# Kernel optimization log

Measured on AMD Instinct MI355X. Metric: run time of the kernel, lower is better.

The kernel has to match this reference:

```python
import jax, jax.numpy as jnp
import numpy as np
import math

V, TB, C, H, L = 50257, 1024, 1024, 16, 8
B, T = 2, 1024
D = C // H


def setup_inputs() -> dict:
    key = jax.random.key(0)
    ks = jax.random.split(key, 16)
    s = 0.02
    n = lambda k, shp: (jax.random.normal(k, shp, jnp.float32) * s)
    inp = {
        "idx": jax.random.randint(ks[0], (B, T), 0, V),
        "tok_emb": n(ks[1], (V, C)),
        "pos_emb": n(ks[2], (1, TB, C)),
        # per-layer stacked params (torch Linear convention: W is [out, in])
        "Wq": n(ks[3], (L, C, C)), "bq": jnp.zeros((L, C)),
        "Wk": n(ks[4], (L, C, C)), "bk": jnp.zeros((L, C)),
        "Wv": n(ks[5], (L, C, C)), "bv": jnp.zeros((L, C)),
        "Wp": n(ks[6], (L, C, C)), "bp": jnp.zeros((L, C)),
        "ln1_w": jnp.ones((L, C)), "ln1_b": jnp.zeros((L, C)),
        "ln2_w": jnp.ones((L, C)), "ln2_b": jnp.zeros((L, C)),
        "W1": n(ks[7], (L, 4 * C, C)), "b1": jnp.zeros((L, 4 * C)),
        "W2": n(ks[8], (L, C, 4 * C)), "b2": jnp.zeros((L, C)),
        "lnf_w": jnp.ones((C,)), "lnf_b": jnp.zeros((C,)),
        "head_w": n(ks[9], (V, C)),
    }
    return inp


def _layer_norm(x, w, b, eps=1e-5):
    mu = x.mean(-1, keepdims=True)
    var = x.var(-1, keepdims=True)
    return (x - mu) * jax.lax.rsqrt(var + eps) * w + b


def _gpt_forward(idx, tok_emb, pos_emb, Wq, bq, Wk, bk, Wv, bv, Wp, bp,
                 ln1_w, ln1_b, ln2_w, ln2_b, W1, b1, W2, b2, lnf_w, lnf_b, head_w):
    b, t = idx.shape
    x = tok_emb[idx] + pos_emb[:, :t, :]  # [B, T, C]; drop = identity (eval)
    causal = jnp.tril(jnp.ones((t, t), dtype=bool))  # [T, T]
    scale = 1.0 / math.sqrt(D)

    def block(x, p):
        (wq, bq_, wk, bk_, wv, bv_, wp, bp_, l1w, l1b, l2w, l2b, w1, b1_, w2, b2_) = p
        h = _layer_norm(x, l1w, l1b)
        q = (h @ wq.T + bq_).reshape(b, t, H, D).transpose(0, 2, 1, 3)  # [B,H,T,D]
        k = (h @ wk.T + bk_).reshape(b, t, H, D).transpose(0, 2, 1, 3)
        v = (h @ wv.T + bv_).reshape(b, t, H, D).transpose(0, 2, 1, 3)
        att = jnp.einsum("bhqd,bhkd->bhqk", q, k) * scale
        att = jnp.where(causal, att, -jnp.inf)
        att = jax.nn.softmax(att, axis=-1)
        y = jnp.einsum("bhqk,bhkd->bhqd", att, v)
        y = y.transpose(0, 2, 1, 3).reshape(b, t, C)
        x = x + (y @ wp.T + bp_)
        h2 = _layer_norm(x, l2w, l2b)
        m = jax.nn.gelu(h2 @ w1.T + b1_, approximate=False)  # torch nn.GELU (erf)
        x = x + (m @ w2.T + b2_)
        return x, None

    params = (Wq, bq, Wk, bk, Wv, bv, Wp, bp, ln1_w, ln1_b, ln2_w, ln2_b, W1, b1, W2, b2)
    x, _ = jax.lax.scan(block, x, params)
    x = _layer_norm(x, lnf_w, lnf_b)
    logits = x @ head_w.T  # [B, T, V]
    return logits


def reference(idx, tok_emb, pos_emb, Wq, bq, Wk, bk, Wv, bv, Wp, bp,
              ln1_w, ln1_b, ln2_w, ln2_b, W1, b1, W2, b2, lnf_w, lnf_b, head_w):
    return _gpt_forward(idx, tok_emb, pos_emb, Wq, bq, Wk, bk, Wv, bv, Wp, bp,
                        ln1_w, ln1_b, ln2_w, ln2_b, W1, b1, W2, b2, lnf_w, lnf_b, head_w)
```

## Files before the change

### kernel.cpp

```cpp
#include <hip/hip_runtime.h>
#include <math.h>

#define V_ 50257
#define C_ 1024
#define H_ 16
#define L_ 8
#define B_ 2
#define T_ 1024
#define BT_ 2048
#define CC_ (C_*C_)
#define QLD_ 3072

typedef unsigned short ushort_t;
using bf16x8 = __attribute__((ext_vector_type(8))) short;
using f32x4  = __attribute__((ext_vector_type(4))) float;

#define AS1 __attribute__((address_space(1)))
#define AS3 __attribute__((address_space(3)))
#define VMCNT0() asm volatile("s_waitcnt vmcnt(0)" ::: "memory")
#define LGKM0()  asm volatile("s_waitcnt lgkmcnt(0)" ::: "memory")
#define RBAR()   asm volatile("s_barrier" ::: "memory")

__device__ __forceinline__ ushort_t f2bf(float f){
  union { float f; unsigned u; } a; a.f = f;
  unsigned r = a.u + 0x7fffu + ((a.u >> 16) & 1u);
  return (ushort_t)(r >> 16);
}

__device__ __forceinline__ unsigned cvtpk_bf16(float a, float b){
  unsigned r;
  asm("v_cvt_pk_bf16_f32 %0, %1, %2" : "=v"(r) : "v"(a), "v"(b));
  return r;
}

__device__ __forceinline__ float wave_sum(float v){
  #pragma unroll
  for(int o=32;o>0;o>>=1) v += __shfl_down(v,o,64);
  return v;
}

__global__ __launch_bounds__(256) void cvt_blk(const float* __restrict__ s, ushort_t* __restrict__ d,
    long inner4, int nblk, long dstStride4){
  long total = inner4 * nblk;
  for(long i = (long)blockIdx.x*256 + threadIdx.x; i < total; i += (long)gridDim.x*256){
    long blk = i / inner4, r = i - blk*inner4;
    float4 v = ((const float4*)s)[i];
    ushort4 o; o.x=f2bf(v.x); o.y=f2bf(v.y); o.z=f2bf(v.z); o.w=f2bf(v.w);
    ((ushort4*)d)[blk*dstStride4 + r] = o;
  }
}

__global__ __launch_bounds__(256) void cvt_qkv(const float* __restrict__ wq,
    const float* __restrict__ wk, const float* __restrict__ wv, ushort_t* __restrict__ d){
  const long inner4 = (long)CC_/4;
  const long total = (long)L_*3*inner4;
  for(long i = (long)blockIdx.x*256 + threadIdx.x; i < total; i += (long)gridDim.x*256){
    long l = i / (3*inner4), r = i - l*3*inner4;
    int which = (int)(r / inner4);
    long rr = r - (long)which*inner4;
    const float* s = (which==0 ? wq : which==1 ? wk : wv) + (l*inner4 + rr)*4;
    float4 v = *(const float4*)s;
    ushort4 o; o.x=f2bf(v.x); o.y=f2bf(v.y); o.z=f2bf(v.z); o.w=f2bf(v.w);
    ((ushort4*)d)[i] = o;
  }
}

__global__ __launch_bounds__(256) void pack_qkv_bias(const float* __restrict__ bq,
    const float* __restrict__ bk, const float* __restrict__ bv, float* __restrict__ dst){
  int i = blockIdx.x*256 + threadIdx.x;
  int l = i / QLD_, c = i - l*QLD_;
  float v;
  if(c < C_)            v = bq[l*C_ + c];
  else if(c < 2*C_)     v = bk[l*C_ + c - C_];
  else                  v = bv[l*C_ + c - 2*C_];
  dst[i] = v;
}

__global__ __launch_bounds__(256) void embed_kernel(const int* __restrict__ idx,
    const float* __restrict__ tok, const float* __restrict__ pos, float* __restrict__ x){
  int i = blockIdx.x*256 + threadIdx.x;
  int c = i & (C_-1); int bt = i >> 10; int t = bt & (T_-1);
  x[i] = tok[(size_t)idx[bt]*C_ + c] + pos[t*C_ + c];
}

__global__ __launch_bounds__(256) void ln_kernel(const float* in, const float* __restrict__ w,
    const float* __restrict__ b, float* outF, ushort_t* outB){
  int row = blockIdx.x;
  const float* xr = in + (size_t)row*C_;
  float vals[4]; float sum=0.f, sq=0.f;
  #pragma unroll
  for(int l=0;l<4;l++){ float v = xr[threadIdx.x + l*256]; vals[l]=v; sum+=v; sq+=v*v; }
  __shared__ float r1[4], r2[4];
  float s1 = wave_sum(sum), s2 = wave_sum(sq);
  int wid = threadIdx.x>>6, lane = threadIdx.x&63;
  if(lane==0){ r1[wid]=s1; r2[wid]=s2; }
  __syncthreads();
  float tot  = r1[0]+r1[1]+r1[2]+r1[3];
  float tot2 = r2[0]+r2[1]+r2[2]+r2[3];
  float mu  = tot * (1.f/C_);
  float var = tot2 * (1.f/C_) - mu*mu;
  float inv = rsqrtf(var + 1e-5f);
  #pragma unroll
  for(int l=0;l<4;l++){
    int c = threadIdx.x + l*256;
    float v = (vals[l]-mu)*inv*w[c] + b[c];
    if(outB) outB[(size_t)row*C_ + c] = f2bf(v);
    else     outF[(size_t)row*C_ + c] = v;
  }
}

template<int BN>
__global__ __launch_bounds__(256) void gemm_mfma(
    const ushort_t* __restrict__ A, const ushort_t* __restrict__ W,
    const float* __restrict__ bias, const float* resid,
    float* outF, ushort_t* outB,
    int M, int N, int K, int act, int nt, int qs)
{
  constexpr int BM = 128;
  constexpr int NSB = BN/16;
  constexpr int NBF = BN/32;
  __shared__ __align__(16) short sA[3][8*512];
  __shared__ __align__(16) short sB[3][NSB*512];
  const int tid  = threadIdx.x;
  const int lane = tid & 63, wid = tid >> 6;
  const int wr = wid >> 1, wc = wid & 1;
  const int nwg = gridDim.x * gridDim.y;
  const int lid = blockIdx.x + gridDim.x * blockIdx.y;
  const int swz = (lid & 7) * (nwg >> 3) + (lid >> 3);
  const int m0 = (swz % gridDim.x) * BM, n0 = (swz / gridDim.x) * BN;
  const int r16 = lane & 15, kq = lane >> 4;

  auto stage = [&](int buf, int k0){
    #pragma unroll
    for(int s2=0; s2<2; ++s2){
      int s = wid*2 + s2;
      const ushort_t* g = A + (size_t)(m0 + s*16 + r16)*K + k0 + kq*8;
      __builtin_amdgcn_global_load_lds((const AS1 void*)g,
          (AS3 void*)&sA[buf][s*512], 16, 0, 0);
    }
    #pragma unroll
    for(int s2=0; s2<NSB/4; ++s2){
      int s = wid*(NSB/4) + s2;
      int gn = n0 + s*16 + r16; if(gn >= N) gn = N-1;
      const ushort_t* g = W + (size_t)gn*K + k0 + kq*8;
      __builtin_amdgcn_global_load_lds((const AS1 void*)g,
          (AS3 void*)&sB[buf][s*512], 16, 0, 0);
    }
  };

  f32x4 acc[4][NBF];
  #pragma unroll
  for(int i=0;i<4;i++)
    #pragma unroll
    for(int j=0;j<NBF;j++) acc[i][j] = (f32x4){0.f,0.f,0.f,0.f};

  const int NT = K >> 5;
  stage(0, 0); stage(1, 32); stage(2, 64);

  int cur = 0;
  for(int t=0; t<NT; ++t){
    if(t+2 < NT){
      if constexpr(BN==128) asm volatile("s_waitcnt vmcnt(8)" ::: "memory");
      else                  asm volatile("s_waitcnt vmcnt(6)" ::: "memory");
    } else if(t+1 < NT){
      if constexpr(BN==128) asm volatile("s_waitcnt vmcnt(4)" ::: "memory");
      else                  asm volatile("s_waitcnt vmcnt(3)" ::: "memory");
    } else {
      VMCNT0();
    }
    RBAR();
    bf16x8 af[4], bfr[NBF];
    #pragma unroll
    for(int m=0;m<4;m++) af[m] = *(const bf16x8*)&sA[cur][(wr*4+m)*512 + lane*8];
    #pragma unroll
    for(int n=0;n<NBF;n++) bfr[n] = *(const bf16x8*)&sB[cur][(wc*NBF+n)*512 + lane*8];
    LGKM0();
    RBAR();
    if(t+3 < NT) stage(cur, (t+3)*32);
    #pragma unroll
    for(int m=0;m<4;m++)
      #pragma unroll
      for(int n=0;n<NBF;n++)
        acc[m][n] = __builtin_amdgcn_mfma_f32_16x16x32_bf16(af[m], bfr[n], acc[m][n], 0, 0, 0);
    cur = (cur==2) ? 0 : cur+1;
  }

  const int colb = n0 + wc*(BN/2);
  #pragma unroll
  for(int m=0;m<4;m++){
    int rowb = m0 + wr*64 + m*16 + kq*4;
    #pragma unroll
    for(int n=0;n<NBF;n++){
      int col = colb + n*16 + r16;
      if(col >= N) continue;
      float bv = bias ? bias[col] : 0.f;
      #pragma unroll
      for(int i=0;i<4;i++){
        int row = rowb + i;
        float v = acc[m][n][i] + bv;
        if(qs && col < C_) v *= 0.125f;
        if(act) v = 0.5f*v*(1.f + erff(v*0.70710678118654752f));
        if(resid) v += resid[(size_t)row*N + col];
        if(outB) outB[(size_t)row*N + col] = f2bf(v);
        else if(nt) __builtin_nontemporal_store(v, &outF[(size_t)row*N + col]);
        else outF[(size_t)row*N + col] = v;
      }
    }
  }
}

__global__ __launch_bounds__(256) void flash_kernel(const ushort_t* __restrict__ qkv,
    ushort_t* __restrict__ y){
  const int tid = threadIdx.x, lane = tid & 63, wid = tid >> 6;
  const int r16 = lane & 15, kq = lane >> 4;
  const int lid = blockIdx.x + 16*blockIdx.y;
  const int swz = (lid & 7)*64 + (lid >> 3);
  const int qt = 15 - (swz & 15), bh = swz >> 4;
  const int b = bh >> 4, h = bh & 15;
  const int q0 = qt*64, qw0 = q0 + wid*16;
  const int qa = qw0 + r16;

  __shared__ __align__(16) short Kt[2][8][512];
  __shared__ __align__(16) short VT[2][64][72];
  __shared__ __align__(16) short Pl[4][16][72];
  __shared__ __align__(16) short Ol[4][16][72];

  const size_t rowQ = (size_t)(b*T_ + qa)*QLD_ + h*64 + kq*8;
  bf16x8 qf0 = *(const bf16x8*)(qkv + rowQ);
  bf16x8 qf1 = *(const bf16x8*)(qkv + rowQ + 32);

  auto stageK = [&](int buf, int jt){
    #pragma unroll
    for(int s2=0;s2<2;s2++){
      int s = wid*2 + s2;
      const ushort_t* g = qkv + (size_t)(b*T_ + jt*64 + (s>>1)*16 + r16)*QLD_
                          + C_ + h*64 + (s&1)*32 + kq*8;
      __builtin_amdgcn_global_load_lds((const AS1 void*)g,
          (AS3 void*)&Kt[buf][s][lane*8], 16, 0, 0);
    }
  };

  f32x4 acc[4];
  #pragma unroll
  for(int t=0;t<4;t++) acc[t] = (f32x4){0.f,0.f,0.f,0.f};
  float m_r = -INFINITY, l_r = 0.f;

  {
    stageK(0, 0);
    const ushort_t* vg = qkv + (size_t)(b*T_ + lane)*QLD_ + 2*C_ + h*64;
    bf16x8 va = *(const bf16x8*)(vg + wid*8);
    bf16x8 vb = *(const bf16x8*)(vg + 32 + wid*8);
    VMCNT0();
    #pragma unroll
    for(int j=0;j<8;j++){ VT[0][wid*8+j][lane]=va[j]; VT[0][32+wid*8+j][lane]=vb[j]; }
    __syncthreads();
  }

  const int njt = qt + 1;
  for(int jt=0; jt<njt; ++jt){
    const int cur = jt & 1;
    const bool more = (jt+1) < njt;
    bf16x8 vr0, vr1;
    if(more){
      stageK(cur^1, jt+1);
      const ushort_t* vg = qkv + (size_t)(b*T_ + (jt+1)*64 + lane)*QLD_ + 2*C_ + h*64;
      vr0 = *(const bf16x8*)(vg + wid*8);
      vr1 = *(const bf16x8*)(vg + 32 + wid*8);
    }

    f32x4 st[4];
    __builtin_amdgcn_s_setprio(1);
    #pragma unroll
    for(int kr=0;kr<4;kr++){
      st[kr] = (f32x4){0.f,0.f,0.f,0.f};
      st[kr] = __builtin_amdgcn_mfma_f32_16x16x32_bf16(*(const bf16x8*)&Kt[cur][kr*2+0][lane*8], qf0, st[kr], 0,0,0);
      st[kr] = __builtin_amdgcn_mfma_f32_16x16x32_bf16(*(const bf16x8*)&Kt[cur][kr*2+1][lane*8], qf1, st[kr], 0,0,0);
    }
    __builtin_amdgcn_s_setprio(0);

    float vals[16];
    if(jt == njt-1){
      #pragma unroll
      for(int kr=0;kr<4;kr++)
        #pragma unroll
        for(int i=0;i<4;i++){
          int ka = jt*64 + kr*16 + 4*kq + i;
          vals[kr*4+i] = (ka <= qa) ? st[kr][i] : -INFINITY;
        }
    } else {
      #pragma unroll
      for(int kr=0;kr<4;kr++)
        #pragma unroll
        for(int i=0;i<4;i++) vals[kr*4+i] = st[kr][i];
    }
    float t8[8];
    #pragma unroll
    for(int i=0;i<8;i++) t8[i] = fmaxf(vals[i], vals[i+8]);
    float t4a = fmaxf(t8[0],t8[4]), t4b = fmaxf(t8[1],t8[5]);
    float t4c = fmaxf(t8[2],t8[6]), t4d = fmaxf(t8[3],t8[7]);
    float pmax = fmaxf(fmaxf(t4a,t4b), fmaxf(t4c,t4d));
    pmax = fmaxf(pmax, __shfl_xor(pmax, 16, 64));
    pmax = fmaxf(pmax, __shfl_xor(pmax, 32, 64));

    if(!__all(pmax - m_r <= 8.f)){
      float mnew = fmaxf(m_r, pmax);
      float alpha = __expf(m_r - mnew);
      l_r *= alpha;
      #pragma unroll
      for(int t=0;t<4;t++)
        #pragma unroll
        for(int j=0;j<4;j++) acc[t][j] *= alpha;
      m_r = mnew;
    }

    float ps = 0.f;
    #pragma unroll
    for(int kr=0;kr<4;kr++){
      float p0 = __expf(vals[kr*4+0]-m_r), p1 = __expf(vals[kr*4+1]-m_r);
      float p2 = __expf(vals[kr*4+2]-m_r), p3 = __expf(vals[kr*4+3]-m_r);
      ps += (p0+p1)+(p2+p3);
      *(unsigned*)&Pl[wid][r16][kr*16 + 4*kq]     = cvtpk_bf16(p0, p1);
      *(unsigned*)&Pl[wid][r16][kr*16 + 4*kq + 2] = cvtpk_bf16(p2, p3);
    }
    ps += __shfl_xor(ps, 16, 64);
    ps += __shfl_xor(ps, 32, 64);
    l_r += ps;

    union { bf16x8 v8; uint2 u2[2]; } pf, vf;
    __builtin_amdgcn_s_setprio(1);
    #pragma unroll
    for(int ks2=0; ks2<2; ks2++){
      pf.u2[0] = *(const uint2*)&Pl[wid][r16][ks2*32 + kq*8];
      pf.u2[1] = *(const uint2*)&Pl[wid][r16][ks2*32 + kq*8 + 4];
      #pragma unroll
      for(int db=0; db<4; db++){
        vf.u2[0] = *(const uint2*)&VT[cur][16*db + r16][ks2*32 + kq*8];
        vf.u2[1] = *(const uint2*)&VT[cur][16*db + r16][ks2*32 + kq*8 + 4];
        acc[db] = __builtin_amdgcn_mfma_f32_16x16x32_bf16(vf.v8, pf.v8, acc[db], 0,0,0);
      }
    }
    __builtin_amdgcn_s_setprio(0);

    if(more){
      VMCNT0();
      #pragma unroll
      for(int j=0;j<8;j++){ VT[cur^1][wid*8+j][lane]=vr0[j]; VT[cur^1][32+wid*8+j][lane]=vr1[j]; }
    }
    __syncthreads();
  }

  float linv = 1.f / l_r;
  #pragma unroll
  for(int db=0; db<4; db++)
    #pragma unroll
    for(int i=0;i<4;i++)
      Ol[wid][r16][16*db + 4*kq + i] = (short)f2bf(acc[db][i]*linv);
  int q = lane >> 2, c0 = (lane & 3)*16;
  const short* src = &Ol[wid][q][c0];
  uint2 a0 = *(const uint2*)(src+0), a1 = *(const uint2*)(src+4);
  uint2 a2 = *(const uint2*)(src+8), a3 = *(const uint2*)(src+12);
  ushort_t* dst = y + (size_t)(b*T_ + qw0 + q)*C_ + h*64 + c0;
  uint4 w0 = {a0.x, a0.y, a1.x, a1.y}, w1 = {a2.x, a2.y, a3.x, a3.y};
  *(uint4*)(dst+0) = w0;
  *(uint4*)(dst+8) = w1;
}

__global__ __launch_bounds__(256) void gemm_nt(const float* __restrict__ A, const float* __restrict__ W,
    const float* __restrict__ bias, const float* resid, float* Cm,
    int M, int N, int K, int act){
  __shared__ float As[16][68];
  __shared__ float Bs[16][68];
  int m0 = blockIdx.y*64, n0 = blockIdx.x*64;
  int tid = threadIdx.x;
  int tx = tid & 15, ty = tid >> 4;
  float acc[4][4] = {};
  for(int k0=0;k0<K;k0+=16){
    #pragma unroll
    for(int l=0;l<4;l++){
      int li = tid + l*256;
      int r = li >> 4, c = li & 15;
      int gm = m0 + r, gn = n0 + r, gk = k0 + c;
      As[c][r] = (gm<M) ? A[(size_t)gm*K + gk] : 0.f;
      Bs[c][r] = (gn<N) ? W[(size_t)gn*K + gk] : 0.f;
    }
    __syncthreads();
    #pragma unroll
    for(int k=0;k<16;k++){
      float4 av = *(const float4*)&As[k][ty*4];
      float4 bv = *(const float4*)&Bs[k][tx*4];
      float a[4] = {av.x, av.y, av.z, av.w};
      float b4[4] = {bv.x, bv.y, bv.z, bv.w};
      #pragma unroll
      for(int i=0;i<4;i++)
        #pragma unroll
        for(int j=0;j<4;j++)
          acc[i][j] = fmaf(a[i], b4[j], acc[i][j]);
    }
    __syncthreads();
  }
  #pragma unroll
  for(int i=0;i<4;i++){
    int m = m0 + ty*4 + i; if(m>=M) continue;
    #pragma unroll
    for(int j=0;j<4;j++){
      int n = n0 + tx*4 + j; if(n>=N) continue;
      float v = acc[i][j];
      if(bias) v += bias[n];
      if(act)  v = 0.5f*v*(1.f + erff(v*0.70710678118654752f));
      if(resid) v += resid[(size_t)m*N + n];
      Cm[(size_t)m*N + n] = v;
    }
  }
}

extern "C" void kernel_launch(void* const* d_in, const int* in_sizes, int n_in,
                              void* d_out, int out_size, void* d_ws, size_t ws_size,
                              hipStream_t stream) {
  const int*   idx  = (const int*)  d_in[0];
  const float* tok  = (const float*)d_in[1];
  const float* pos  = (const float*)d_in[2];
  const float* Wq   = (const float*)d_in[3];
  const float* bq   = (const float*)d_in[4];
  const float* Wk   = (const float*)d_in[5];
  const float* bk   = (const float*)d_in[6];
  const float* Wv   = (const float*)d_in[7];
  const float* bv   = (const float*)d_in[8];
  const float* Wp   = (const float*)d_in[9];
  const float* bp   = (const float*)d_in[10];
  const float* ln1w = (const float*)d_in[11];
  const float* ln1b = (const float*)d_in[12];
  const float* ln2w = (const float*)d_in[13];
  const float* ln2b = (const float*)d_in[14];
  const float* W1   = (const float*)d_in[15];
  const float* b1   = (const float*)d_in[16];
  const float* W2   = (const float*)d_in[17];
  const float* b2   = (const float*)d_in[18];
  const float* lnfw = (const float*)d_in[19];
  const float* lnfb = (const float*)d_in[20];
  const float* headw= (const float*)d_in[21];

  float* out = (float*)d_out;
  ushort_t* qkvb = (ushort_t*)(out);
  ushort_t* hb   = (ushort_t*)(out + 3145728);
  ushort_t* yb   = (ushort_t*)(out + 4194304);
  ushort_t* mb   = (ushort_t*)(out + 5242880);
  ushort_t* wqkv = (ushort_t*)(out + 9437184);
  ushort_t* wpb  = (ushort_t*)(out + 22020096);
  ushort_t* w1b  = (ushort_t*)(out + 26214400);
  ushort_t* w2b  = (ushort_t*)(out + 42991616);
  float*    bqkv = out + 59768832;
  float*    x    = (float*)d_ws;
  ushort_t* xb   = (ushort_t*)((float*)d_ws + 2097152);
  ushort_t* whb  = (ushort_t*)((float*)d_ws + 3145728);
  const bool big = ws_size >= (size_t)28877312 * 4;

  cvt_qkv<<<4096,256,0,stream>>>(Wq, Wk, Wv, wqkv);
  cvt_blk<<<2048,256,0,stream>>>(Wp, wpb,  (long)L_*CC_/4,   1, (long)L_*CC_/4);
  cvt_blk<<<2048,256,0,stream>>>(W1, w1b,  (long)L_*CC_,     1, (long)L_*CC_);
  cvt_blk<<<2048,256,0,stream>>>(W2, w2b,  (long)L_*CC_,     1, (long)L_*CC_);
  if(big) cvt_blk<<<2048,256,0,stream>>>(headw, whb, (long)V_*C_/4, 1, (long)V_*C_/4);
  pack_qkv_bias<<<L_*QLD_/256,256,0,stream>>>(bq, bk, bv, bqkv);

  embed_kernel<<<BT_*C_/256, 256, 0, stream>>>(idx, tok, pos, x);

  for(int l=0;l<L_;l++){
    ln_kernel<<<BT_,256,0,stream>>>(x, ln1w + l*C_, ln1b + l*C_, nullptr, hb);
    gemm_mfma<128><<<dim3(BT_/128, QLD_/128),256,0,stream>>>(hb, wqkv + (size_t)l*3*CC_,
        bqkv + l*QLD_, nullptr, nullptr, qkvb, BT_, QLD_, C_, 0, 0, 1);
    flash_kernel<<<dim3(T_/64, B_*H_),256,0,stream>>>(qkvb, yb);
    gemm_mfma<64><<<dim3(BT_/128, C_/64),256,0,stream>>>(yb, wpb + (size_t)l*CC_,
        bp + l*C_, x, x, nullptr, BT_, C_, C_, 0, 0, 0);
    ln_kernel<<<BT_,256,0,stream>>>(x, ln2w + l*C_, ln2b + l*C_, nullptr, hb);
    gemm_mfma<128><<<dim3(BT_/128, 4*C_/128),256,0,stream>>>(hb, w1b + (size_t)l*4*CC_,
        b1 + (size_t)l*4*C_, nullptr, nullptr, mb, BT_, 4*C_, C_, 1, 0, 0);
    gemm_mfma<64><<<dim3(BT_/128, C_/64),256,0,stream>>>(mb, w2b + (size_t)l*4*CC_,
        b2 + l*C_, x, x, nullptr, BT_, C_, 4*C_, 0, 0, 0);
  }

  if(big){
    ln_kernel<<<BT_,256,0,stream>>>(x, lnfw, lnfb, nullptr, xb);
    gemm_mfma<128><<<dim3(BT_/128, (V_+127)/128),256,0,stream>>>(xb, whb,
        nullptr, nullptr, out, nullptr, BT_, V_, C_, 0, 1, 0);
  } else {
    ln_kernel<<<BT_,256,0,stream>>>(x, lnfw, lnfb, x, nullptr);
    gemm_nt<<<dim3((V_+63)/64, BT_/64),256,0,stream>>>(x, headw, nullptr, nullptr, out,
                                                       BT_, V_, C_, 0);
  }
}
```

Baseline: 2.728 ms.

## Add 64-row-tile triple-buffered MFMA GEMM for per-layer projections

Introduces a new GEMM kernel with 64-row M tiles, a K step of 32, and a three-stage global-to-LDS pipeline that uses direct global_load_lds and explicit vmcnt waits. The QKV, output projection, MLP up and MLP down GEMMs in every layer now use it in place of the 128-row-tile kernel. Smaller M tiles double the number of workgroups, which is meant to fill the MI355X compute units better on these mid-sized GEMMs and hide load latency through deeper prefetch. The cost is less operand reuse per tile and more total global traffic for the weight matrix.

```diff
diff --git a/kernel.cpp b/kernel.cpp
--- a/kernel.cpp
+++ b/kernel.cpp
@@ -203,6 +203,101 @@
         if(resid) v += resid[(size_t)row*N + col];
         if(outB) outB[(size_t)row*N + col] = f2bf(v);
         else if(nt) __builtin_nontemporal_store(v, &outF[(size_t)row*N + col]);
+        else outF[(size_t)row*N + col] = v;
+      }
+    }
+  }
+}
+
+template<int BN>
+__global__ __launch_bounds__(256) void gemm_s64(
+    const ushort_t* __restrict__ A, const ushort_t* __restrict__ W,
+    const float* __restrict__ bias, const float* resid,
+    float* outF, ushort_t* outB,
+    int M, int N, int K, int act, int qs)
+{
+  constexpr int NSB = BN/16;
+  constexpr int NBF = BN/32;
+  constexpr int LPW = 1 + NSB/4;
+  __shared__ __align__(16) short sA[3][4*512];
+  __shared__ __align__(16) short sB[3][NSB*512];
+  const int tid  = threadIdx.x;
+  const int lane = tid & 63, wid = tid >> 6;
+  const int wr = wid >> 1, wc = wid & 1;
+  const int nwg = gridDim.x * gridDim.y;
+  const int lid = blockIdx.x + gridDim.x * blockIdx.y;
+  const int swz = (lid & 7) * (nwg >> 3) + (lid >> 3);
+  const int m0 = (swz % gridDim.x) * 64, n0 = (swz / gridDim.x) * BN;
+  const int r16 = lane & 15, kq = lane >> 4;
+
+  auto stage = [&](int buf, int k0){
+    {
+      const ushort_t* g = A + (size_t)(m0 + wid*16 + r16)*K + k0 + kq*8;
+      __builtin_amdgcn_global_load_lds((const AS1 void*)g,
+          (AS3 void*)&sA[buf][wid*512], 16, 0, 0);
+    }
+    #pragma unroll
+    for(int s2=0; s2<NSB/4; ++s2){
+      int s = wid*(NSB/4) + s2;
+      const ushort_t* g = W + (size_t)(n0 + s*16 + r16)*K + k0 + kq*8;
+      __builtin_amdgcn_global_load_lds((const AS1 void*)g,
+          (AS3 void*)&sB[buf][s*512], 16, 0, 0);
+    }
+  };
+
+  f32x4 acc[2][NBF];
+  #pragma unroll
+  for(int i=0;i<2;i++)
+    #pragma unroll
+    for(int j=0;j<NBF;j++) acc[i][j] = (f32x4){0.f,0.f,0.f,0.f};
+
+  const int NT = K >> 5;
+  stage(0, 0); stage(1, 32); stage(2, 64);
+
+  int cur = 0;
+  for(int t=0; t<NT; ++t){
+    if(t+2 < NT){
+      if constexpr(LPW==2) asm volatile("s_waitcnt vmcnt(4)" ::: "memory");
+      else                 asm volatile("s_waitcnt vmcnt(6)" ::: "memory");
+    } else if(t+1 < NT){
+      if constexpr(LPW==2) asm volatile("s_waitcnt vmcnt(2)" ::: "memory");
+      else                 asm volatile("s_waitcnt vmcnt(3)" ::: "memory");
+    } else {
+      VMCNT0();
+    }
+    RBAR();
+    bf16x8 af[2], bfr[NBF];
+    #pragma unroll
+    for(int m=0;m<2;m++) af[m] = *(const bf16x8*)&sA[cur][(wr*2+m)*512 + lane*8];
+    #pragma unroll
+    for(int n=0;n<NBF;n++) bfr[n] = *(const bf16x8*)&sB[cur][(wc*NBF+n)*512 + lane*8];
+    LGKM0();
+    RBAR();
+    if(t+3 < NT) stage(cur, (t+3)*32);
+    #pragma unroll
+    for(int m=0;m<2;m++)
+      #pragma unroll
+      for(int n=0;n<NBF;n++)
+        acc[m][n] = __builtin_amdgcn_mfma_f32_16x16x32_bf16(af[m], bfr[n], acc[m][n], 0, 0, 0);
+    cur = (cur==2) ? 0 : cur+1;
+  }
+
+  const int colb = n0 + wc*(BN/2);
+  #pragma unroll
+  for(int m=0;m<2;m++){
+    int rowb = m0 + wr*32 + m*16 + kq*4;
+    #pragma unroll
+    for(int n=0;n<NBF;n++){
+      int col = colb + n*16 + r16;
+      float bv = bias ? bias[col] : 0.f;
+      #pragma unroll
+      for(int i=0;i<4;i++){
+        int row = rowb + i;
+        float v = acc[m][n][i] + bv;
+        if(qs && col < C_) v *= 0.125f;
+        if(act) v = 0.5f*v*(1.f + erff(v*0.70710678118654752f));
+        if(resid) v += resid[(size_t)row*N + col];
+        if(outB) outB[(size_t)row*N + col] = f2bf(v);
         else outF[(size_t)row*N + col] = v;
       }
     }
@@ -465,16 +560,16 @@
 
   for(int l=0;l<L_;l++){
     ln_kernel<<<BT_,256,0,stream>>>(x, ln1w + l*C_, ln1b + l*C_, nullptr, hb);
-    gemm_mfma<128><<<dim3(BT_/128, QLD_/128),256,0,stream>>>(hb, wqkv + (size_t)l*3*CC_,
-        bqkv + l*QLD_, nullptr, nullptr, qkvb, BT_, QLD_, C_, 0, 0, 1);
+    gemm_s64<128><<<dim3(BT_/64, QLD_/128),256,0,stream>>>(hb, wqkv + (size_t)l*3*CC_,
+        bqkv + l*QLD_, nullptr, nullptr, qkvb, BT_, QLD_, C_, 0, 1);
     flash_kernel<<<dim3(T_/64, B_*H_),256,0,stream>>>(qkvb, yb);
-    gemm_mfma<64><<<dim3(BT_/128, C_/64),256,0,stream>>>(yb, wpb + (size_t)l*CC_,
-        bp + l*C_, x, x, nullptr, BT_, C_, C_, 0, 0, 0);
+    gemm_s64<64><<<dim3(BT_/64, C_/64),256,0,stream>>>(yb, wpb + (size_t)l*CC_,
+        bp + l*C_, x, x, nullptr, BT_, C_, C_, 0, 0);
     ln_kernel<<<BT_,256,0,stream>>>(x, ln2w + l*C_, ln2b + l*C_, nullptr, hb);
-    gemm_mfma<128><<<dim3(BT_/128, 4*C_/128),256,0,stream>>>(hb, w1b + (size_t)l*4*CC_,
-        b1 + (size_t)l*4*C_, nullptr, nullptr, mb, BT_, 4*C_, C_, 1, 0, 0);
-    gemm_mfma<64><<<dim3(BT_/128, C_/64),256,0,stream>>>(mb, w2b + (size_t)l*4*CC_,
-        b2 + l*C_, x, x, nullptr, BT_, C_, 4*C_, 0, 0, 0);
+    gemm_s64<128><<<dim3(BT_/64, 4*C_/128),256,0,stream>>>(hb, w1b + (size_t)l*4*CC_,
+        b1 + (size_t)l*4*C_, nullptr, nullptr, mb, BT_, 4*C_, C_, 1, 0);
+    gemm_s64<64><<<dim3(BT_/64, C_/64),256,0,stream>>>(mb, w2b + (size_t)l*4*CC_,
+        b2 + l*C_, x, x, nullptr, BT_, C_, 4*C_, 0, 0);
   }
 
   if(big){
```

Measured after the change: 2.667 ms. 2.2% less time.
